# Kernel optimization log

Hardware: AMD Instinct MI355X
Metric: run time of the kernel (lower is better)

The kernel has to match this reference:

```python
import jax, jax.numpy as jnp
import numpy as np

DIM = 384
HEADS = 6
NEG = -1e9  # masked-score fill; equivalent to gathering only kept K/V rows


def setup_inputs() -> dict:
    key = jax.random.key(0)
    ks = jax.random.split(key, 9)
    B, N, C = 1, 4098, DIM
    x = jax.random.normal(ks[0], (B, N, C), dtype=jnp.float32)
    pos = jax.random.normal(ks[1], (B, N + 1, C), dtype=jnp.float32)
    # float mask in [0,1); >=0.5 means 'foreground / keep as key', <0.5 pooled into back token
    mask = jax.random.uniform(ks[2], (B, 1, N - 2), dtype=jnp.float32)
    mask_block = jnp.ones((N + 1,), dtype=jnp.float32)  # positions 0, N-1, N always kept
    Wq = jax.random.normal(ks[3], (C, C), dtype=jnp.float32) * 0.02
    Wk = jax.random.normal(ks[4], (C, C), dtype=jnp.float32) * 0.02
    Wv = jax.random.normal(ks[5], (C, C), dtype=jnp.float32) * 0.02
    Wp = jax.random.normal(ks[6], (C, C), dtype=jnp.float32) * 0.02
    bp = jnp.zeros((C,), dtype=jnp.float32)
    return {"x": x, "pos": pos, "mask": mask, "mask_block": mask_block,
            "Wq": Wq, "Wk": Wk, "Wv": Wv, "Wp": Wp, "bp": bp}


def reference(x, pos, mask, mask_block, Wq, Wk, Wv, Wp, bp):
    B, N, C = x.shape
    H = HEADS
    D = C // H
    scale = D ** -0.5
    eps = 1e-10

    # back token: average of background (mask < 0.5) interior tokens
    reverse = jnp.where(mask < 0.5, 1.0, 0.0)                      # (B,1,N-2)
    pooled = jnp.einsum('bon,bnc->boc', reverse, x[:, 1:N - 1])    # (B,1,C)
    back_tokens = pooled / (reverse.sum(axis=2, keepdims=True) + eps)

    kv_x = jnp.concatenate([x, back_tokens], axis=1)               # (B,N+1,C)
    q_x = x + pos[:, :N]
    k_x = kv_x + pos

    q = (q_x @ Wq.T).reshape(B, N, H, D).transpose(0, 2, 1, 3)       # (B,H,N,D)
    k = (k_x @ Wk.T).reshape(B, N + 1, H, D).transpose(0, 2, 1, 3)   # (B,H,N+1,D)
    v = (kv_x @ Wv.T).reshape(B, N + 1, H, D).transpose(0, 2, 1, 3)  # (B,H,N+1,D)

    # key-selection mask: original gathers rows with mask_block >= 0.5;
    # masked softmax over all N+1 keys is mathematically identical.
    mb = mask_block.at[1:N - 1].set(mask[0, 0])
    keep = mb >= 0.5                                               # (N+1,)

    scores = jnp.einsum('bhqd,bhkd->bhqk', q, k) * scale
    scores = jnp.where(keep[None, None, None, :], scores, NEG)
    attn = jax.nn.softmax(scores, axis=-1)
    out = jnp.einsum('bhqk,bhkd->bhqd', attn, v)
    out = out.transpose(0, 2, 1, 3).reshape(B, N, C)
    return out @ Wp.T + bp
```

## Files before the change

kernel.cpp:

```cpp
#include <hip/hip_runtime.h>
#include <math.h>

#define N_TOK 4098
#define NK_TOK 4099
#define C_DIM 384
#define NKPAD 4160
#define NSLICE 6

typedef short  bh8 __attribute__((ext_vector_type(8)));
typedef float  f32x4 __attribute__((ext_vector_type(4)));
typedef unsigned short ushort;
typedef ushort u4 __attribute__((ext_vector_type(4)));
typedef ushort u8 __attribute__((ext_vector_type(8)));

static __device__ __forceinline__ ushort f2bf(float f) {
  unsigned int u = __float_as_uint(f);
  u = (u + 0x7FFF + ((u >> 16) & 1)) >> 16;
  return (ushort)u;
}
static __device__ __forceinline__ float bf2f(ushort s) {
  return __uint_as_float(((unsigned int)s) << 16);
}

#define QSCALE 0.18033688011112042f

__global__ __launch_bounds__(384) void pool_kernel(
    const float* __restrict__ x, const float* __restrict__ mask,
    float* __restrict__ pooled_part, float* __restrict__ cnt_part) {
  const int b = blockIdx.x, t = threadIdx.x;
  const int r0 = b * 32;
  float acc = 0.f;
  int lc = 0;
  for (int r = r0; r < r0 + 32; ++r)
    if (mask[r] < 0.5f) { acc += x[(size_t)(r + 1) * C_DIM + t]; ++lc; }
  pooled_part[b * C_DIM + t] = acc;
  if (t == 0) cnt_part[b] = (float)lc;
}

__global__ __launch_bounds__(256) void prep_kernel(
    const float* __restrict__ x, const float* __restrict__ pos,
    const float* __restrict__ pooled_part, const float* __restrict__ cnt_part,
    const float* __restrict__ Wq, const float* __restrict__ Wk,
    const float* __restrict__ Wv, const float* __restrict__ Wp,
    const float* __restrict__ mask, const float* __restrict__ mask_block,
    ushort* __restrict__ Aq, ushort* __restrict__ Ak, ushort* __restrict__ Av,
    ushort* __restrict__ Wb, int* __restrict__ nk, int* __restrict__ inv) {
  const int b = blockIdx.x, t = threadIdx.x;
  if (b < 260) {
    __shared__ float sback[C_DIM];
    if (b == 256) {
      float cs = 0.f;
      for (int i = (t & 63); i < 128; i += 64) cs += cnt_part[i];
#pragma unroll
      for (int d = 1; d < 64; d <<= 1) cs += __shfl_xor(cs, d);
      const float ic = 1.f / (cs + 1e-10f);
      for (int c = t; c < C_DIM; c += 256) {
        float s = 0.f;
        for (int p = 0; p < 128; ++p) s += pooled_part[p * C_DIM + c];
        sback[c] = s * ic;
      }
      __syncthreads();
    }
    const int r0 = b * 16;
#pragma unroll
    for (int i = 0; i < 6; ++i) {
      const int idx = i * 1024 + t * 4;
      const int row = r0 + idx / C_DIM, col = idx % C_DIM;
      if (row >= NK_TOK) continue;
      const float4 pv = *(const float4*)&pos[(size_t)row * C_DIM + col];
      float4 xv;
      if (row == NK_TOK - 1)
        xv = make_float4(sback[col], sback[col + 1], sback[col + 2], sback[col + 3]);
      else
        xv = *(const float4*)&x[(size_t)row * C_DIM + col];
      if (row < N_TOK) {
        u4 q4 = {f2bf((xv.x + pv.x) * QSCALE), f2bf((xv.y + pv.y) * QSCALE),
                 f2bf((xv.z + pv.z) * QSCALE), f2bf((xv.w + pv.w) * QSCALE)};
        *(u4*)&Aq[(size_t)row * C_DIM + col] = q4;
      }
      u4 k4 = {f2bf(xv.x + pv.x), f2bf(xv.y + pv.y),
               f2bf(xv.z + pv.z), f2bf(xv.w + pv.w)};
      *(u4*)&Ak[(size_t)row * C_DIM + col] = k4;
      u4 v4 = {f2bf(xv.x), f2bf(xv.y), f2bf(xv.z), f2bf(xv.w)};
      *(u4*)&Av[(size_t)row * C_DIM + col] = v4;
    }
  } else if (b < 292) {
    const int wi = b - 260;
    const float* src = (wi < 8) ? Wq : (wi < 16) ? Wk : (wi < 24) ? Wv : Wp;
    const int base = (wi >> 3) * 147456 + (wi & 7) * 18432;
#pragma unroll 2
    for (int i = 0; i < 18; ++i) {
      const int g = base + i * 1024 + t * 4;
      const float4 v = *(const float4*)&src[(wi & 7) * 18432 + i * 1024 + t * 4];
      u4 o = {f2bf(v.x), f2bf(v.y), f2bf(v.z), f2bf(v.w)};
      *(u4*)&Wb[g] = o;
    }
  } else {
    __shared__ int scnt[256];
    const int j0 = t * 17;
    unsigned int bits = 0;
    int c = 0;
#pragma unroll 1
    for (int u = 0; u < 17; ++u) {
      const int j = j0 + u;
      bool keep = false;
      if (j < NK_TOK)
        keep = (j >= 1 && j <= N_TOK - 2) ? (mask[j - 1] >= 0.5f)
                                          : (mask_block[j] >= 0.5f);
      if (keep) { bits |= 1u << u; ++c; }
    }
    scnt[t] = c;
    __syncthreads();
    for (int d = 1; d < 256; d <<= 1) {
      const int v = scnt[t];
      const int add = (t >= d) ? scnt[t - d] : 0;
      __syncthreads();
      scnt[t] = v + add;
      __syncthreads();
    }
    int base = scnt[t] - c;
    if (t == 255) *nk = scnt[255];
#pragma unroll 1
    for (int u = 0; u < 17; ++u) {
      const int j = j0 + u;
      if (j < NK_TOK) inv[j] = ((bits >> u) & 1) ? base++ : -1;
    }
  }
}

static __device__ __forceinline__ void gemm_core(
    const ushort* __restrict__ A, const ushort* __restrict__ B,
    ushort (* __restrict__ As)[72], ushort (* __restrict__ Bs)[72],
    int t, int w, int quad, int l15, f32x4 acc[4]) {
  const int g = t & 7;
  u8 ra[2], rb[2];
#pragma unroll
  for (int it = 0; it < 2; ++it) {
    const int r = it * 32 + (t >> 3);
    ra[it] = *(const u8*)&A[r * C_DIM + g * 8];
    rb[it] = *(const u8*)&B[r * C_DIM + g * 8];
  }
#pragma unroll 1
  for (int kt = 0; kt < 6; ++kt) {
    __syncthreads();
#pragma unroll
    for (int it = 0; it < 2; ++it) {
      const int r = it * 32 + (t >> 3);
      *(u8*)&As[r][g * 8] = ra[it];
      *(u8*)&Bs[r][g * 8] = rb[it];
    }
    __syncthreads();
    if (kt < 5) {
      const int k0 = (kt + 1) * 64;
#pragma unroll
      for (int it = 0; it < 2; ++it) {
        const int r = it * 32 + (t >> 3);
        ra[it] = *(const u8*)&A[r * C_DIM + k0 + g * 8];
        rb[it] = *(const u8*)&B[r * C_DIM + k0 + g * 8];
      }
    }
    const bh8 b0 = *(const bh8*)&Bs[w * 16 + l15][quad * 8];
    const bh8 b1 = *(const bh8*)&Bs[w * 16 + l15][32 + quad * 8];
#pragma unroll
    for (int mb = 0; mb < 4; ++mb) {
      const bh8 a0 = *(const bh8*)&As[mb * 16 + l15][quad * 8];
      const bh8 a1 = *(const bh8*)&As[mb * 16 + l15][32 + quad * 8];
      acc[mb] = __builtin_amdgcn_mfma_f32_16x16x32_bf16(a0, b0, acc[mb], 0, 0, 0);
      acc[mb] = __builtin_amdgcn_mfma_f32_16x16x32_bf16(a1, b1, acc[mb], 0, 0, 0);
    }
  }
}

__global__ __launch_bounds__(256) void gemm3_kernel(
    const ushort* __restrict__ Aq, const ushort* __restrict__ Ak,
    const ushort* __restrict__ Av, const ushort* __restrict__ Wb,
    const int* __restrict__ inv, ushort* __restrict__ Qh,
    ushort* __restrict__ Kc, ushort* __restrict__ Vt) {
  __shared__ ushort As[64][72], Bs[64][72];
  const int t = threadIdx.x, w = t >> 6, lane = t & 63;
  const int quad = lane >> 4, l15 = lane & 15;
  const int m0 = blockIdx.x * 64;
  const int which = blockIdx.y / 6, h = blockIdx.y % 6;
  const ushort* A = (which == 0 ? Aq : which == 1 ? Ak : Av) + (size_t)m0 * C_DIM;
  const ushort* B = Wb + (size_t)which * 147456 + (size_t)h * 64 * C_DIM;
  f32x4 acc[4];
#pragma unroll
  for (int i = 0; i < 4; ++i) acc[i] = (f32x4){0.f, 0.f, 0.f, 0.f};
  gemm_core(A, B, As, Bs, t, w, quad, l15, acc);
  const int n = w * 16 + l15;
  if (which == 0) {
#pragma unroll
    for (int mb = 0; mb < 4; ++mb)
#pragma unroll
      for (int r = 0; r < 4; ++r) {
        const int m = m0 + mb * 16 + quad * 4 + r;
        if (m < N_TOK) Qh[((size_t)h * N_TOK + m) * 64 + n] = f2bf(acc[mb][r]);
      }
  } else if (which == 1) {
#pragma unroll
    for (int mb = 0; mb < 4; ++mb)
#pragma unroll
      for (int r = 0; r < 4; ++r) {
        const int m = m0 + mb * 16 + quad * 4 + r;
        if (m < NK_TOK) {
          const int slot = inv[m];
          if (slot >= 0) Kc[((size_t)h * NKPAD + slot) * 64 + n] = f2bf(acc[mb][r]);
        }
      }
  } else {
#pragma unroll
    for (int mb = 0; mb < 4; ++mb)
#pragma unroll
      for (int r = 0; r < 4; ++r) {
        const int m = m0 + mb * 16 + quad * 4 + r;
        if (m < NK_TOK) {
          const int slot = inv[m];
          if (slot >= 0) Vt[((size_t)h * 64 + n) * NKPAD + slot] = f2bf(acc[mb][r]);
        }
      }
  }
}

__global__ __launch_bounds__(256) void gemm_out_kernel(
    const ushort* __restrict__ Am, const ushort* __restrict__ Wpb,
    const float* __restrict__ bp, float* __restrict__ out) {
  __shared__ ushort As[64][72], Bs[64][72];
  const int t = threadIdx.x, w = t >> 6, lane = t & 63;
  const int quad = lane >> 4, l15 = lane & 15;
  const int m0 = blockIdx.x * 64;
  const int h = blockIdx.y;
  f32x4 acc[4];
#pragma unroll
  for (int i = 0; i < 4; ++i) acc[i] = (f32x4){0.f, 0.f, 0.f, 0.f};
  gemm_core(Am + (size_t)m0 * C_DIM, Wpb + (size_t)h * 64 * C_DIM,
            As, Bs, t, w, quad, l15, acc);
  const int n = w * 16 + l15;
  const float bb = bp[h * 64 + n];
#pragma unroll
  for (int mb = 0; mb < 4; ++mb)
#pragma unroll
    for (int r = 0; r < 4; ++r) {
      const int m = m0 + mb * 16 + quad * 4 + r;
      if (m < N_TOK) out[(size_t)m * C_DIM + h * 64 + n] = acc[mb][r] + bb;
    }
}

__global__ __launch_bounds__(256) void attn_kernel(
    const ushort* __restrict__ Qh, const ushort* __restrict__ Kc,
    const ushort* __restrict__ Vt, const int* __restrict__ nkp,
    ushort* __restrict__ Opart, float* __restrict__ Lpart) {
  __shared__ ushort Ks[64][72];
  __shared__ ushort Vs[64][72];
  __shared__ ushort Ps[4][32][72];
  const int t = threadIdx.x, w = t >> 6, lane = t & 63;
  const int quad = lane >> 4, l15 = lane & 15;
  const int h = blockIdx.y, slice = blockIdx.z;
  const int q0 = blockIdx.x * 128;
  const int nk = *nkp, nchunk = (nk + 63) >> 6;
  const int g = t & 7;

  bh8 qf[2][2];
#pragma unroll
  for (int qa = 0; qa < 2; ++qa) {
    int qr = q0 + w * 32 + qa * 16 + l15;
    if (qr > N_TOK - 1) qr = N_TOK - 1;
    const ushort* qp = Qh + ((size_t)h * N_TOK + qr) * 64 + quad * 8;
    qf[qa][0] = *(const bh8*)qp;
    qf[qa][1] = *(const bh8*)(qp + 32);
  }
  f32x4 oacc[2][4];
#pragma unroll
  for (int qa = 0; qa < 2; ++qa)
#pragma unroll
    for (int i = 0; i < 4; ++i) oacc[qa][i] = (f32x4){0.f, 0.f, 0.f, 0.f};
  float l_r[2] = {0.f, 0.f};

  const ushort* kb = Kc + (size_t)h * NKPAD * 64;
  const ushort* vb = Vt + (size_t)h * 64 * NKPAD;

  const ushort* kstage = kb + ((size_t)slice * 64 + (t >> 3)) * 64 + g * 8;
  const ushort* vstage = vb + (size_t)(t >> 3) * NKPAD + slice * 64 + g * 8;

  u8 rk[2], rv[2];
  if (slice < nchunk) {
    rk[0] = *(const u8*)kstage;
    rk[1] = *(const u8*)(kstage + 32 * 64);
    rv[0] = *(const u8*)vstage;
    rv[1] = *(const u8*)(vstage + (size_t)32 * NKPAD);
  }
#pragma unroll 1
  for (int kc = slice; kc < nchunk; kc += NSLICE) {
    __syncthreads();
    {
      const int r = t >> 3;
      *(u8*)&Ks[r][g * 8] = rk[0];
      *(u8*)&Ks[32 + r][g * 8] = rk[1];
      *(u8*)&Vs[r][g * 8] = rv[0];
      *(u8*)&Vs[32 + r][g * 8] = rv[1];
    }
    __syncthreads();
    if (kc + NSLICE < nchunk) {
      kstage += NSLICE * 64 * 64;
      vstage += NSLICE * 64;
      rk[0] = *(const u8*)kstage;
      rk[1] = *(const u8*)(kstage + 32 * 64);
      rv[0] = *(const u8*)vstage;
      rv[1] = *(const u8*)(vstage + (size_t)32 * NKPAD);
    }
    float csum[2] = {0.f, 0.f};
#pragma unroll
    for (int f = 0; f < 4; ++f) {
      const bh8 a0 = *(const bh8*)&Ks[f * 16 + l15][quad * 8];
      const bh8 a1 = *(const bh8*)&Ks[f * 16 + l15][32 + quad * 8];
      f32x4 s4[2];
#pragma unroll
      for (int qa = 0; qa < 2; ++qa) {
        s4[qa] = (f32x4){0.f, 0.f, 0.f, 0.f};
        s4[qa] = __builtin_amdgcn_mfma_f32_16x16x32_bf16(a0, qf[qa][0], s4[qa], 0, 0, 0);
        s4[qa] = __builtin_amdgcn_mfma_f32_16x16x32_bf16(a1, qf[qa][1], s4[qa], 0, 0, 0);
      }
      const int keyb = kc * 64 + f * 16 + quad * 4;
#pragma unroll
      for (int qa = 0; qa < 2; ++qa) {
        const float p0 = (keyb + 0 < nk) ? __builtin_amdgcn_exp2f(s4[qa][0]) : 0.f;
        const float p1 = (keyb + 1 < nk) ? __builtin_amdgcn_exp2f(s4[qa][1]) : 0.f;
        const float p2 = (keyb + 2 < nk) ? __builtin_amdgcn_exp2f(s4[qa][2]) : 0.f;
        const float p3 = (keyb + 3 < nk) ? __builtin_amdgcn_exp2f(s4[qa][3]) : 0.f;
        csum[qa] += (p0 + p1) + (p2 + p3);
        unsigned int lo, hi;
        asm("v_cvt_pk_bf16_f32 %0, %1, %2" : "=v"(lo) : "v"(p0), "v"(p1));
        asm("v_cvt_pk_bf16_f32 %0, %1, %2" : "=v"(hi) : "v"(p2), "v"(p3));
        uint2 pk;
        pk.x = lo; pk.y = hi;
        *(uint2*)&Ps[w][qa * 16 + l15][f * 16 + quad * 4] = pk;
      }
    }
#pragma unroll
    for (int qa = 0; qa < 2; ++qa) {
      csum[qa] += __shfl_xor(csum[qa], 16);
      csum[qa] += __shfl_xor(csum[qa], 32);
      l_r[qa] += csum[qa];
    }

    bh8 pa[2][2];
#pragma unroll
    for (int qa = 0; qa < 2; ++qa) {
      pa[qa][0] = *(const bh8*)&Ps[w][qa * 16 + l15][quad * 8];
      pa[qa][1] = *(const bh8*)&Ps[w][qa * 16 + l15][32 + quad * 8];
    }
#pragma unroll
    for (int db = 0; db < 4; ++db) {
      const bh8 b0 = *(const bh8*)&Vs[db * 16 + l15][quad * 8];
      const bh8 b1 = *(const bh8*)&Vs[db * 16 + l15][32 + quad * 8];
#pragma unroll
      for (int qa = 0; qa < 2; ++qa) {
        oacc[qa][db] = __builtin_amdgcn_mfma_f32_16x16x32_bf16(pa[qa][0], b0, oacc[qa][db], 0, 0, 0);
        oacc[qa][db] = __builtin_amdgcn_mfma_f32_16x16x32_bf16(pa[qa][1], b1, oacc[qa][db], 0, 0, 0);
      }
    }
  }

  const int sh = slice * 6 + h;
#pragma unroll
  for (int qa = 0; qa < 2; ++qa) {
    const int qg = q0 + w * 32 + qa * 16;
#pragma unroll
    for (int db = 0; db < 4; ++db)
#pragma unroll
      for (int r = 0; r < 4; ++r) {
        const int q = qg + quad * 4 + r;
        if (q < N_TOK)
          Opart[((size_t)sh * NKPAD + q) * 64 + db * 16 + l15] = f2bf(oacc[qa][db][r]);
      }
    if (quad == 0) {
      const int q = qg + l15;
      if (q < N_TOK) Lpart[sh * NKPAD + q] = l_r[qa];
    }
  }
}

__global__ __launch_bounds__(256) void merge_kernel(const ushort* __restrict__ Opart,
                                                    const float* __restrict__ Lpart,
                                                    ushort* __restrict__ Am) {
  const int idx = blockIdx.x * 256 + threadIdx.x;
  if (idx >= N_TOK * 48) return;
  const int q = idx / 48, c = (idx % 48) * 8;
  const int h = c >> 6, d = c & 63;
  float l = 0.f;
#pragma unroll
  for (int s = 0; s < NSLICE; ++s) l += Lpart[(s * 6 + h) * NKPAD + q];
  const float inv = 1.f / l;
  float o[8] = {0.f, 0.f, 0.f, 0.f, 0.f, 0.f, 0.f, 0.f};
#pragma unroll
  for (int s = 0; s < NSLICE; ++s) {
    const u8 v = *(const u8*)&Opart[((size_t)(s * 6 + h) * NKPAD + q) * 64 + d];
#pragma unroll
    for (int j = 0; j < 8; ++j) o[j] += bf2f(v[j]);
  }
  u8 r;
#pragma unroll
  for (int j = 0; j < 8; ++j) r[j] = f2bf(o[j] * inv);
  *(u8*)&Am[(size_t)q * C_DIM + c] = r;
}

extern "C" void kernel_launch(void* const* d_in, const int* in_sizes, int n_in,
                              void* d_out, int out_size, void* d_ws, size_t ws_size,
                              hipStream_t stream) {
  const float* x          = (const float*)d_in[0];
  const float* pos        = (const float*)d_in[1];
  const float* mask       = (const float*)d_in[2];
  const float* mask_block = (const float*)d_in[3];
  const float* Wq         = (const float*)d_in[4];
  const float* Wk         = (const float*)d_in[5];
  const float* Wv         = (const float*)d_in[6];
  const float* Wp         = (const float*)d_in[7];
  const float* bp         = (const float*)d_in[8];
  float* out = (float*)d_out;
  char* wsb = (char*)d_ws;

  float*  pooled_part = (float*)wsb;
  float*  cnt_part    = (float*)(wsb + 196608);
  int*    nk          = (int*)(wsb + 197120);
  int*    inv         = (int*)(wsb + 197632);
  ushort* Aq          = (ushort*)(wsb + 215296);
  ushort* Ak          = (ushort*)(wsb + 3410176);
  ushort* Av          = (ushort*)(wsb + 6605056);
  ushort* Wb          = (ushort*)(wsb + 9799936);
  ushort* Qh          = (ushort*)(wsb + 10979584);
  ushort* Kc          = (ushort*)(wsb + 14126848);
  ushort* Vt          = (ushort*)(wsb + 17321728);
  ushort* Am          = (ushort*)(wsb + 24011008);
  ushort* Op          = (ushort*)(wsb + 27205888);
  float*  Lp          = (float*)(wsb + 46375168);

  pool_kernel<<<dim3(128), dim3(384), 0, stream>>>(x, mask, pooled_part, cnt_part);
  prep_kernel<<<dim3(293), dim3(256), 0, stream>>>(x, pos, pooled_part, cnt_part,
                                                   Wq, Wk, Wv, Wp, mask, mask_block,
                                                   Aq, Ak, Av, Wb, nk, inv);
  gemm3_kernel<<<dim3(65, 18), 256, 0, stream>>>(Aq, Ak, Av, Wb, inv, Qh, Kc, Vt);
  attn_kernel<<<dim3(33, 6, NSLICE), 256, 0, stream>>>(Qh, Kc, Vt, nk, Op, Lp);
  merge_kernel<<<dim3(769), 256, 0, stream>>>(Op, Lp, Am);
  gemm_out_kernel<<<dim3(65, 6), 256, 0, stream>>>(Am, Wb + 3 * 147456, bp, out);
}
```

Before: 152.8 us.

## Double query rows per attention block to reuse K/V tiles across more queries

Each wave now processes 64 query rows instead of 32, so a block covers 256 queries and the grid shrinks from 33 to 17 blocks along the query axis. Every staged K/V chunk in shared memory feeds twice as many MFMAs, halving redundant K/V global loads and LDS staging per query. The cost is more accumulator and Q registers, a larger P buffer in shared memory, and only 612 blocks in total, which may reduce occupancy and leave CUs underused.

```diff
diff --git a/kernel.cpp b/kernel.cpp
--- a/kernel.cpp
+++ b/kernel.cpp
@@ -251,29 +251,29 @@
     ushort* __restrict__ Opart, float* __restrict__ Lpart) {
   __shared__ ushort Ks[64][72];
   __shared__ ushort Vs[64][72];
-  __shared__ ushort Ps[4][32][72];
+  __shared__ ushort Ps[4][64][72];
   const int t = threadIdx.x, w = t >> 6, lane = t & 63;
   const int quad = lane >> 4, l15 = lane & 15;
   const int h = blockIdx.y, slice = blockIdx.z;
-  const int q0 = blockIdx.x * 128;
+  const int q0 = blockIdx.x * 256;
   const int nk = *nkp, nchunk = (nk + 63) >> 6;
   const int g = t & 7;
 
-  bh8 qf[2][2];
-#pragma unroll
-  for (int qa = 0; qa < 2; ++qa) {
-    int qr = q0 + w * 32 + qa * 16 + l15;
+  bh8 qf[4][2];
+#pragma unroll
+  for (int qa = 0; qa < 4; ++qa) {
+    int qr = q0 + w * 64 + qa * 16 + l15;
     if (qr > N_TOK - 1) qr = N_TOK - 1;
     const ushort* qp = Qh + ((size_t)h * N_TOK + qr) * 64 + quad * 8;
     qf[qa][0] = *(const bh8*)qp;
     qf[qa][1] = *(const bh8*)(qp + 32);
   }
-  f32x4 oacc[2][4];
-#pragma unroll
-  for (int qa = 0; qa < 2; ++qa)
+  f32x4 oacc[4][4];
+#pragma unroll
+  for (int qa = 0; qa < 4; ++qa)
 #pragma unroll
     for (int i = 0; i < 4; ++i) oacc[qa][i] = (f32x4){0.f, 0.f, 0.f, 0.f};
-  float l_r[2] = {0.f, 0.f};
+  float l_r[4] = {0.f, 0.f, 0.f, 0.f};
 
   const ushort* kb = Kc + (size_t)h * NKPAD * 64;
   const ushort* vb = Vt + (size_t)h * 64 * NKPAD;
@@ -307,25 +307,21 @@
       rv[0] = *(const u8*)vstage;
       rv[1] = *(const u8*)(vstage + (size_t)32 * NKPAD);
     }
-    float csum[2] = {0.f, 0.f};
+    float csum[4] = {0.f, 0.f, 0.f, 0.f};
 #pragma unroll
     for (int f = 0; f < 4; ++f) {
       const bh8 a0 = *(const bh8*)&Ks[f * 16 + l15][quad * 8];
       const bh8 a1 = *(const bh8*)&Ks[f * 16 + l15][32 + quad * 8];
-      f32x4 s4[2];
-#pragma unroll
-      for (int qa = 0; qa < 2; ++qa) {
-        s4[qa] = (f32x4){0.f, 0.f, 0.f, 0.f};
-        s4[qa] = __builtin_amdgcn_mfma_f32_16x16x32_bf16(a0, qf[qa][0], s4[qa], 0, 0, 0);
-        s4[qa] = __builtin_amdgcn_mfma_f32_16x16x32_bf16(a1, qf[qa][1], s4[qa], 0, 0, 0);
-      }
       const int keyb = kc * 64 + f * 16 + quad * 4;
 #pragma unroll
-      for (int qa = 0; qa < 2; ++qa) {
-        const float p0 = (keyb + 0 < nk) ? __builtin_amdgcn_exp2f(s4[qa][0]) : 0.f;
-        const float p1 = (keyb + 1 < nk) ? __builtin_amdgcn_exp2f(s4[qa][1]) : 0.f;
-        const float p2 = (keyb + 2 < nk) ? __builtin_amdgcn_exp2f(s4[qa][2]) : 0.f;
-        const float p3 = (keyb + 3 < nk) ? __builtin_amdgcn_exp2f(s4[qa][3]) : 0.f;
+      for (int qa = 0; qa < 4; ++qa) {
+        f32x4 s4 = {0.f, 0.f, 0.f, 0.f};
+        s4 = __builtin_amdgcn_mfma_f32_16x16x32_bf16(a0, qf[qa][0], s4, 0, 0, 0);
+        s4 = __builtin_amdgcn_mfma_f32_16x16x32_bf16(a1, qf[qa][1], s4, 0, 0, 0);
+        const float p0 = (keyb + 0 < nk) ? __builtin_amdgcn_exp2f(s4[0]) : 0.f;
+        const float p1 = (keyb + 1 < nk) ? __builtin_amdgcn_exp2f(s4[1]) : 0.f;
+        const float p2 = (keyb + 2 < nk) ? __builtin_amdgcn_exp2f(s4[2]) : 0.f;
+        const float p3 = (keyb + 3 < nk) ? __builtin_amdgcn_exp2f(s4[3]) : 0.f;
         csum[qa] += (p0 + p1) + (p2 + p3);
         unsigned int lo, hi;
         asm("v_cvt_pk_bf16_f32 %0, %1, %2" : "=v"(lo) : "v"(p0), "v"(p1));
@@ -336,34 +332,34 @@
       }
     }
 #pragma unroll
-    for (int qa = 0; qa < 2; ++qa) {
+    for (int qa = 0; qa < 4; ++qa) {
       csum[qa] += __shfl_xor(csum[qa], 16);
       csum[qa] += __shfl_xor(csum[qa], 32);
       l_r[qa] += csum[qa];
     }
 
-    bh8 pa[2][2];
-#pragma unroll
-    for (int qa = 0; qa < 2; ++qa) {
-      pa[qa][0] = *(const bh8*)&Ps[w][qa * 16 + l15][quad * 8];
-      pa[qa][1] = *(const bh8*)&Ps[w][qa * 16 + l15][32 + quad * 8];
+    bh8 pa0[4], pa1[4];
+#pragma unroll
+    for (int qa = 0; qa < 4; ++qa) {
+      pa0[qa] = *(const bh8*)&Ps[w][qa * 16 + l15][quad * 8];
+      pa1[qa] = *(const bh8*)&Ps[w][qa * 16 + l15][32 + quad * 8];
     }
 #pragma unroll
     for (int db = 0; db < 4; ++db) {
       const bh8 b0 = *(const bh8*)&Vs[db * 16 + l15][quad * 8];
       const bh8 b1 = *(const bh8*)&Vs[db * 16 + l15][32 + quad * 8];
 #pragma unroll
-      for (int qa = 0; qa < 2; ++qa) {
-        oacc[qa][db] = __builtin_amdgcn_mfma_f32_16x16x32_bf16(pa[qa][0], b0, oacc[qa][db], 0, 0, 0);
-        oacc[qa][db] = __builtin_amdgcn_mfma_f32_16x16x32_bf16(pa[qa][1], b1, oacc[qa][db], 0, 0, 0);
+      for (int qa = 0; qa < 4; ++qa) {
+        oacc[qa][db] = __builtin_amdgcn_mfma_f32_16x16x32_bf16(pa0[qa], b0, oacc[qa][db], 0, 0, 0);
+        oacc[qa][db] = __builtin_amdgcn_mfma_f32_16x16x32_bf16(pa1[qa], b1, oacc[qa][db], 0, 0, 0);
       }
     }
   }
 
   const int sh = slice * 6 + h;
 #pragma unroll
-  for (int qa = 0; qa < 2; ++qa) {
-    const int qg = q0 + w * 32 + qa * 16;
+  for (int qa = 0; qa < 4; ++qa) {
+    const int qg = q0 + w * 64 + qa * 16;
 #pragma unroll
     for (int db = 0; db < 4; ++db)
 #pragma unroll
@@ -438,7 +434,7 @@
                                                    Wq, Wk, Wv, Wp, mask, mask_block,
                                                    Aq, Ak, Av, Wb, nk, inv);
   gemm3_kernel<<<dim3(65, 18), 256, 0, stream>>>(Aq, Ak, Av, Wb, inv, Qh, Kc, Vt);
-  attn_kernel<<<dim3(33, 6, NSLICE), 256, 0, stream>>>(Qh, Kc, Vt, nk, Op, Lp);
+  attn_kernel<<<dim3(17, 6, NSLICE), 256, 0, stream>>>(Qh, Kc, Vt, nk, Op, Lp);
   merge_kernel<<<dim3(769), 256, 0, stream>>>(Op, Lp, Am);
   gemm_out_kernel<<<dim3(65, 6), 256, 0, stream>>>(Am, Wb + 3 * 147456, bp, out);
 }
```

Result: slower. 160.3 us (+5.0%).

## Double-buffer shared-memory tiles in GEMM core and halve attention slice count

Applied to the files above, without the earlier changes.

The GEMM mainloop now ping-pongs between two shared-memory buffers for the A and B tiles. This removes one of the two barriers per k-step and lets the global prefetch of the next tile overlap with the MFMA work on the current one. NSLICE also drops from 6 to 3, which changes the split used by the attention kernel (not visible here) and likely reduces parallelism while cutting merge overhead. Doubling shared memory per block may lower occupancy.

```diff
diff --git a/kernel.cpp b/kernel.cpp
--- a/kernel.cpp
+++ b/kernel.cpp
@@ -5,7 +5,7 @@
 #define NK_TOK 4099
 #define C_DIM 384
 #define NKPAD 4160
-#define NSLICE 6
+#define NSLICE 3
 
 typedef short  bh8 __attribute__((ext_vector_type(8)));
 typedef float  f32x4 __attribute__((ext_vector_type(4)));
@@ -130,43 +130,48 @@
 
 static __device__ __forceinline__ void gemm_core(
     const ushort* __restrict__ A, const ushort* __restrict__ B,
-    ushort (* __restrict__ As)[72], ushort (* __restrict__ Bs)[72],
+    ushort (* __restrict__ As)[64][72], ushort (* __restrict__ Bs)[64][72],
     int t, int w, int quad, int l15, f32x4 acc[4]) {
   const int g = t & 7;
+  const int r = t >> 3;
   u8 ra[2], rb[2];
 #pragma unroll
   for (int it = 0; it < 2; ++it) {
-    const int r = it * 32 + (t >> 3);
-    ra[it] = *(const u8*)&A[r * C_DIM + g * 8];
-    rb[it] = *(const u8*)&B[r * C_DIM + g * 8];
+    ra[it] = *(const u8*)&A[(it * 32 + r) * C_DIM + g * 8];
+    rb[it] = *(const u8*)&B[(it * 32 + r) * C_DIM + g * 8];
+  }
+#pragma unroll
+  for (int it = 0; it < 2; ++it) {
+    *(u8*)&As[0][it * 32 + r][g * 8] = ra[it];
+    *(u8*)&Bs[0][it * 32 + r][g * 8] = rb[it];
   }
 #pragma unroll 1
   for (int kt = 0; kt < 6; ++kt) {
-    __syncthreads();
-#pragma unroll
-    for (int it = 0; it < 2; ++it) {
-      const int r = it * 32 + (t >> 3);
-      *(u8*)&As[r][g * 8] = ra[it];
-      *(u8*)&Bs[r][g * 8] = rb[it];
-    }
-    __syncthreads();
     if (kt < 5) {
       const int k0 = (kt + 1) * 64;
 #pragma unroll
       for (int it = 0; it < 2; ++it) {
-        const int r = it * 32 + (t >> 3);
-        ra[it] = *(const u8*)&A[r * C_DIM + k0 + g * 8];
-        rb[it] = *(const u8*)&B[r * C_DIM + k0 + g * 8];
-      }
-    }
-    const bh8 b0 = *(const bh8*)&Bs[w * 16 + l15][quad * 8];
-    const bh8 b1 = *(const bh8*)&Bs[w * 16 + l15][32 + quad * 8];
+        ra[it] = *(const u8*)&A[(it * 32 + r) * C_DIM + k0 + g * 8];
+        rb[it] = *(const u8*)&B[(it * 32 + r) * C_DIM + k0 + g * 8];
+      }
+    }
+    __syncthreads();
+    const int cb = kt & 1;
+    const bh8 b0 = *(const bh8*)&Bs[cb][w * 16 + l15][quad * 8];
+    const bh8 b1 = *(const bh8*)&Bs[cb][w * 16 + l15][32 + quad * 8];
 #pragma unroll
     for (int mb = 0; mb < 4; ++mb) {
-      const bh8 a0 = *(const bh8*)&As[mb * 16 + l15][quad * 8];
-      const bh8 a1 = *(const bh8*)&As[mb * 16 + l15][32 + quad * 8];
+      const bh8 a0 = *(const bh8*)&As[cb][mb * 16 + l15][quad * 8];
+      const bh8 a1 = *(const bh8*)&As[cb][mb * 16 + l15][32 + quad * 8];
       acc[mb] = __builtin_amdgcn_mfma_f32_16x16x32_bf16(a0, b0, acc[mb], 0, 0, 0);
       acc[mb] = __builtin_amdgcn_mfma_f32_16x16x32_bf16(a1, b1, acc[mb], 0, 0, 0);
+    }
+    if (kt < 5) {
+#pragma unroll
+      for (int it = 0; it < 2; ++it) {
+        *(u8*)&As[cb ^ 1][it * 32 + r][g * 8] = ra[it];
+        *(u8*)&Bs[cb ^ 1][it * 32 + r][g * 8] = rb[it];
+      }
     }
   }
 }
@@ -176,7 +181,7 @@
     const ushort* __restrict__ Av, const ushort* __restrict__ Wb,
     const int* __restrict__ inv, ushort* __restrict__ Qh,
     ushort* __restrict__ Kc, ushort* __restrict__ Vt) {
-  __shared__ ushort As[64][72], Bs[64][72];
+  __shared__ ushort As[2][64][72], Bs[2][64][72];
   const int t = threadIdx.x, w = t >> 6, lane = t & 63;
   const int quad = lane >> 4, l15 = lane & 15;
   const int m0 = blockIdx.x * 64;
@@ -224,7 +229,7 @@
 __global__ __launch_bounds__(256) void gemm_out_kernel(
     const ushort* __restrict__ Am, const ushort* __restrict__ Wpb,
     const float* __restrict__ bp, float* __restrict__ out) {
-  __shared__ ushort As[64][72], Bs[64][72];
+  __shared__ ushort As[2][64][72], Bs[2][64][72];
   const int t = threadIdx.x, w = t >> 6, lane = t & 63;
   const int quad = lane >> 4, l15 = lane & 15;
   const int m0 = blockIdx.x * 64;
```

Result: no change. 154.8 us (+1.3%).
